# Kernel tuning notes

Measured on AMD Instinct MI355X. Metric: run time of the kernel, lower is better.

Reference implementation:

```python
import jax, jax.numpy as jnp
import numpy as np

WS = 8        # window_size
NH = 16       # num_heads

def setup_inputs() -> dict:
    key = jax.random.key(0)
    ks = jax.random.split(key, 6)
    B, H, W, C = 16, 64, 64, 512
    nW = (H // WS) * (W // WS)
    return {
        "x": jax.random.normal(ks[0], (B, H * W, C), jnp.float32),
        "qkv_w": jax.random.normal(ks[1], (3 * C, C), jnp.float32) * 0.02,
        "qkv_b": jax.random.normal(ks[2], (3 * C,), jnp.float32) * 0.02,
        "proj_w": jax.random.normal(ks[3], (C, C), jnp.float32) * 0.02,
        "proj_b": jax.random.normal(ks[4], (C,), jnp.float32) * 0.02,
        "attn_mask": jax.random.normal(ks[5], (nW, WS * WS, WS * WS), jnp.float32),
        "H": H,
        "W": W,
    }

def reference(x, qkv_w, qkv_b, proj_w, proj_b, attn_mask, H, W):
    B, N, C = x.shape
    ws = WS
    hd = C // NH
    scale = hd ** (-0.5)
    x_img = x.reshape(B, H, W, C)
    pad_h = (ws - H % ws) % ws
    pad_w = (ws - W % ws) % ws
    if pad_h > 0 or pad_w > 0:
        x_img = jnp.pad(x_img, ((0, 0), (0, pad_h), (0, pad_w), (0, 0)))
    Hp, Wp = H + pad_h, W + pad_w
    nW = (Hp // ws) * (Wp // ws)
    # window partition: [B*nW, ws*ws, C]
    x_win = x_img.reshape(B, Hp // ws, ws, Wp // ws, ws, C)
    x_win = x_win.transpose(0, 1, 3, 2, 4, 5).reshape(B * nW, ws * ws, C)
    # fused qkv projection (torch Linear: y = x @ W^T + b)
    qkv = x_win @ qkv_w.T + qkv_b
    qkv = qkv.reshape(B * nW, ws * ws, 3, NH, hd).transpose(2, 0, 3, 1, 4)
    q, k, v = qkv[0], qkv[1], qkv[2]  # each [B*nW, NH, ws*ws, hd]
    attn = jnp.einsum('bhqd,bhkd->bhqk', q, k) * scale
    if attn_mask is not None:
        attn = attn.reshape(B, nW, NH, ws * ws, ws * ws)
        attn = attn + attn_mask[None, :, None, :, :]
        attn = attn.reshape(B * nW, NH, ws * ws, ws * ws)
    attn = jax.nn.softmax(attn, axis=-1)
    out = jnp.einsum('bhqk,bhkd->bhqd', attn, v)
    out = out.transpose(0, 2, 1, 3).reshape(B * nW, ws * ws, C)
    out = out @ proj_w.T + proj_b
    # window reverse
    out = out.reshape(B, Hp // ws, Wp // ws, ws, ws, C)
    out = out.transpose(0, 1, 3, 2, 4, 5).reshape(B, Hp, Wp, C)
    out = out[:, :H, :W, :].reshape(B, H * W, C)
    return out
```

## Files before the change

kernel.cpp:

```cpp
#include <hip/hip_runtime.h>


typedef unsigned short u16;
typedef unsigned int u32;
typedef __attribute__((ext_vector_type(8))) u16 u16x8;
typedef __attribute__((ext_vector_type(8))) short short8;
typedef __attribute__((ext_vector_type(4))) float f32x4;

__device__ __forceinline__ u16 f2bf(float f) {
    u32 u = __float_as_uint(f);
    u += 0x7fffu + ((u >> 16) & 1u);
    return (u16)(u >> 16);
}

__device__ __forceinline__ f32x4 MFMA(u16x8 a, u16x8 b, f32x4 c) {
    return __builtin_amdgcn_mfma_f32_16x16x32_bf16(
        __builtin_bit_cast(short8, a), __builtin_bit_cast(short8, b), c, 0, 0, 0);
}

__device__ __forceinline__ void gload16(const void* g, void* l) {
    __builtin_amdgcn_global_load_lds(
        (const __attribute__((address_space(1))) void*)g,
        (__attribute__((address_space(3))) void*)l, 16, 0, 0);
}

__device__ __forceinline__ int win2img(int r) {
    int b = r >> 12;
    int w = (r >> 6) & 63;
    int t = r & 63;
    int img = (((w >> 3) << 3) + (t >> 3)) * 64 + ((w & 7) << 3) + (t & 7);
    return (b << 12) + img;
}

__device__ __forceinline__ u16x8 cvt8(const float* src) {
    float4 a = *(const float4*)src;
    float4 b = *(const float4*)(src + 4);
    u16x8 t;
    t[0] = f2bf(a.x); t[1] = f2bf(a.y); t[2] = f2bf(a.z); t[3] = f2bf(a.w);
    t[4] = f2bf(b.x); t[5] = f2bf(b.y); t[6] = f2bf(b.z); t[7] = f2bf(b.w);
    return t;
}

__global__ __launch_bounds__(256)
void conv_f2b(const float* __restrict__ in, u16* __restrict__ out, int n8) {
    int u = blockIdx.x * 256 + threadIdx.x;
    if (u >= n8) return;
    *(u16x8*)(out + (size_t)u * 8) = cvt8(in + (size_t)u * 8);
}

__global__ __launch_bounds__(256)
void conv_permute_x(const float* __restrict__ x, u16* __restrict__ xw) {
    int u = blockIdx.x * 256 + threadIdx.x;
    int r = u >> 6;
    int c = (u & 63) << 3;
    int g = win2img(r);
    *(u16x8*)(xw + (size_t)r * 512 + c) = cvt8(x + (size_t)g * 512 + c);
}

template<bool PERM_OUT, bool OUT_F32>
__global__ __launch_bounds__(256, 2)
void gemm_bt(const u16* __restrict__ A, const u16* __restrict__ Wt,
             const float* __restrict__ bias, void* __restrict__ C, int Nfull)
{
    __shared__ u16 sA[128 * 32];
    __shared__ u16 sB[128 * 32];

    const int tid  = threadIdx.x;
    const int lane = tid & 63;
    const int wv   = tid >> 6;
    const int wm   = (wv >> 1) << 6;
    const int wn   = (wv & 1) << 6;
    const int lr   = lane & 15;
    const int lg   = lane >> 4;
    const int m0   = blockIdx.x * 128;
    const int n0   = blockIdx.y * 128;

    const int grow  = tid >> 2;
    const int gcolb = (tid & 3) << 4;
    const u32 tb    = (u32)tid * 16;

    const char* aptr = (const char*)A + (((size_t)(m0 + grow)) << 10) + gcolb;
    const char* bptr = (const char*)Wt + (((size_t)(n0 + grow)) << 10) + gcolb;
    char* sAb = (char*)sA;
    char* sBb = (char*)sB;

    f32x4 acc[4][4] = {};

    for (int kt = 0; kt < 16; ++kt) {
        __syncthreads();
        const int ko = kt * 64;
        gload16(aptr + ko,              sAb + tb);
        gload16(aptr + (64 << 10) + ko, sAb + 4096 + tb);
        gload16(bptr + ko,              sBb + tb);
        gload16(bptr + (64 << 10) + ko, sBb + 4096 + tb);
        __syncthreads();

        u16x8 af[4], bfr[4];
#pragma unroll
        for (int mi = 0; mi < 4; ++mi)
            af[mi] = *(const u16x8*)(sA + (wm + mi * 16 + lr) * 32 + lg * 8);
#pragma unroll
        for (int ni = 0; ni < 4; ++ni)
            bfr[ni] = *(const u16x8*)(sB + (wn + ni * 16 + lr) * 32 + lg * 8);
#pragma unroll
        for (int mi = 0; mi < 4; ++mi)
#pragma unroll
            for (int ni = 0; ni < 4; ++ni)
                acc[mi][ni] = MFMA(af[mi], bfr[ni], acc[mi][ni]);
    }

#pragma unroll
    for (int mi = 0; mi < 4; ++mi) {
#pragma unroll
        for (int ni = 0; ni < 4; ++ni) {
            const int col = n0 + wn + ni * 16 + lr;
            const float bv = bias[col];
#pragma unroll
            for (int r = 0; r < 4; ++r) {
                int gr = m0 + wm + mi * 16 + lg * 4 + r;
                if (PERM_OUT) gr = win2img(gr);
                const float v = acc[mi][ni][r] + bv;
                if constexpr (OUT_F32)
                    ((float*)C)[(size_t)gr * Nfull + col] = v;
                else
                    ((u16*)C)[(size_t)gr * Nfull + col] = f2bf(v);
            }
        }
    }
}

__global__ __launch_bounds__(256, 2)
void attn_kernel(const u16* __restrict__ qkv, const float* __restrict__ mask,
                 u16* __restrict__ attn_out)
{
    __shared__ u16 sP[4][64][72];

    const int tid  = threadIdx.x;
    const int lane = tid & 63;
    const int wv   = tid >> 6;
    const int lr   = lane & 15;
    const int lg   = lane >> 4;
    const int win  = blockIdx.x;
    const int wib  = win & 63;
    const size_t rb = (size_t)win * 64;
    const float* maskp = mask + (size_t)wib * 64 * 64;
    const float scale = 0.17677669529663687f;

    for (int hi = 0; hi < 4; ++hi) {
        const int h = hi * 4 + wv;
        const size_t hoff = (size_t)h * 32;

        u16x8 qf[4], kf[4];
#pragma unroll
        for (int mt = 0; mt < 4; ++mt) {
            const u16* rowp = qkv + (rb + mt * 16 + lr) * 1536 + hoff + lg * 8;
            qf[mt] = *(const u16x8*)rowp;
            kf[mt] = *(const u16x8*)(rowp + 512);
        }
        f32x4 s[4][4] = {};
#pragma unroll
        for (int mi = 0; mi < 4; ++mi)
#pragma unroll
            for (int ni = 0; ni < 4; ++ni)
                s[mi][ni] = MFMA(qf[mi], kf[ni], s[mi][ni]);

        float rsum[4][4];
#pragma unroll
        for (int mi = 0; mi < 4; ++mi) {
#pragma unroll
            for (int r = 0; r < 4; ++r) {
                const int qrow = mi * 16 + lg * 4 + r;
                float vv[4];
                float mx = -1e30f;
#pragma unroll
                for (int ni = 0; ni < 4; ++ni) {
                    const int kcol = ni * 16 + lr;
                    float v = s[mi][ni][r] * scale + maskp[qrow * 64 + kcol];
                    vv[ni] = v;
                    mx = fmaxf(mx, v);
                }
#pragma unroll
                for (int mk = 1; mk <= 8; mk <<= 1)
                    mx = fmaxf(mx, __shfl_xor(mx, mk, 64));
                float sum = 0.f;
#pragma unroll
                for (int ni = 0; ni < 4; ++ni) {
                    float p = __expf(vv[ni] - mx);
                    sum += p;
                    s[mi][ni][r] = p;
                }
#pragma unroll
                for (int mk = 1; mk <= 8; mk <<= 1)
                    sum += __shfl_xor(sum, mk, 64);
                rsum[mi][r] = sum;
            }
        }

        __syncthreads();
#pragma unroll
        for (int mi = 0; mi < 4; ++mi)
#pragma unroll
            for (int ni = 0; ni < 4; ++ni)
#pragma unroll
                for (int r = 0; r < 4; ++r)
                    sP[wv][mi * 16 + lg * 4 + r][ni * 16 + lr] = f2bf(s[mi][ni][r]);
        __syncthreads();

        u16x8 pf[4][2];
#pragma unroll
        for (int mt = 0; mt < 4; ++mt)
#pragma unroll
            for (int k2 = 0; k2 < 2; ++k2)
                pf[mt][k2] = *(const u16x8*)&sP[wv][mt * 16 + lr][k2 * 32 + lg * 8];

        u16x8 vf[2][2];
#pragma unroll
        for (int k2 = 0; k2 < 2; ++k2)
#pragma unroll
            for (int nt = 0; nt < 2; ++nt) {
                const u16* vp = qkv + (rb + k2 * 32 + lg * 8) * 1536 + 1024 + hoff + nt * 16 + lr;
                u16x8 tmp;
#pragma unroll
                for (int j = 0; j < 8; ++j) tmp[j] = vp[(size_t)j * 1536];
                vf[k2][nt] = tmp;
            }

        f32x4 o[4][2] = {};
#pragma unroll
        for (int mt = 0; mt < 4; ++mt)
#pragma unroll
            for (int k2 = 0; k2 < 2; ++k2)
#pragma unroll
                for (int nt = 0; nt < 2; ++nt)
                    o[mt][nt] = MFMA(pf[mt][k2], vf[k2][nt], o[mt][nt]);

#pragma unroll
        for (int mt = 0; mt < 4; ++mt)
#pragma unroll
            for (int nt = 0; nt < 2; ++nt)
#pragma unroll
                for (int r = 0; r < 4; ++r) {
                    const int row = mt * 16 + lg * 4 + r;
                    const int d = nt * 16 + lr;
                    attn_out[(rb + row) * 512 + hoff + d] =
                        f2bf(o[mt][nt][r] / rsum[mt][r]);
                }
    }
}

extern "C" void kernel_launch(void* const* d_in, const int* in_sizes, int n_in,
                              void* d_out, int out_size, void* d_ws, size_t ws_size,
                              hipStream_t stream)
{
    const float* x      = (const float*)d_in[0];
    const float* qkv_w  = (const float*)d_in[1];
    const float* qkv_b  = (const float*)d_in[2];
    const float* proj_w = (const float*)d_in[3];
    const float* proj_b = (const float*)d_in[4];
    const float* mask   = (const float*)d_in[5];
    float* out = (float*)d_out;

    const size_t WQKV = 1536ull * 512;
    const size_t WPROJ = 512ull * 512;

    u16* wq = (u16*)d_ws;
    u16* wp = wq + WQKV;
    u16* chunk = wp + WPROJ;

    const size_t xwPB  = 4096ull * 512;
    const size_t qkvPB = 4096ull * 1536;
    const size_t attPB = 4096ull * 512;
    const size_t perBatchBytes = (xwPB + qkvPB + attPB) * 2;

    size_t avail = ws_size - (WQKV + WPROJ) * 2;
    int Bc = (int)(avail / perBatchBytes);
    if (Bc > 16) Bc = 16;
    if (Bc < 1) Bc = 1;

    u16* xw_ws  = chunk;
    u16* qkv_ws = xw_ws + (size_t)Bc * xwPB;
    u16* att_ws = qkv_ws + (size_t)Bc * qkvPB;

    conv_f2b<<<dim3((WQKV / 8 + 255) / 256), 256, 0, stream>>>(qkv_w, wq, (int)(WQKV / 8));
    conv_f2b<<<dim3((WPROJ / 8 + 255) / 256), 256, 0, stream>>>(proj_w, wp, (int)(WPROJ / 8));

    for (int b0 = 0; b0 < 16; b0 += Bc) {
        const int bc = (16 - b0) < Bc ? (16 - b0) : Bc;
        const float* xc = x + (size_t)b0 * 4096 * 512;
        float* outc = out + (size_t)b0 * 4096 * 512;

        conv_permute_x<<<dim3(bc * 1024), 256, 0, stream>>>(xc, xw_ws);
        gemm_bt<false, false><<<dim3(bc * 32, 12), 256, 0, stream>>>(
            xw_ws, wq, qkv_b, qkv_ws, 1536);
        attn_kernel<<<dim3(bc * 64), 256, 0, stream>>>(qkv_ws, mask, att_ws);
        gemm_bt<true, true><<<dim3(bc * 32, 4), 256, 0, stream>>>(
            att_ws, wp, proj_b, outc, 512);
    }
}
```

Baseline: 349.0 us.

## Double-buffer GEMM LDS tiles and remap blocks across XCDs with 1D grid

The GEMM kernel now double-buffers its A/B tiles in LDS, so the global-to-LDS load for the next k-step is issued before the MFMAs on the current one, and each step needs one barrier instead of two. The launch is flattened to a 1D grid, and block ids are remapped so that consecutive tiles land on the same XCD (blockIdx mod 8), which should improve L2 reuse of shared A rows. Launch bounds are raised to 4 waves-per-SIMD occupancy. This uses twice the LDS per block and adds register pressure, which could limit the higher occupancy target or cause spills. The remap assumes the grid size is divisible by 8.

Measured after the change: 332.0 us. 1.05x faster.

```diff
diff --git a/kernel.cpp b/kernel.cpp
--- a/kernel.cpp
+++ b/kernel.cpp
@@ -58,12 +58,18 @@
 }
 
 template<bool PERM_OUT, bool OUT_F32>
-__global__ __launch_bounds__(256, 2)
+__global__ __launch_bounds__(256, 4)
 void gemm_bt(const u16* __restrict__ A, const u16* __restrict__ Wt,
-             const float* __restrict__ bias, void* __restrict__ C, int Nfull)
+             const float* __restrict__ bias, void* __restrict__ C,
+             int NB, int Nfull)
 {
-    __shared__ u16 sA[128 * 32];
-    __shared__ u16 sB[128 * 32];
+    __shared__ char lds[32768];
+
+    const int nwg = gridDim.x;
+    const int q   = nwg >> 3;
+    const int wg  = (blockIdx.x & 7) * q + (blockIdx.x >> 3);
+    const int m0  = (wg / NB) * 128;
+    const int n0  = (wg % NB) * 128;
 
     const int tid  = threadIdx.x;
     const int lane = tid & 63;
@@ -72,42 +78,57 @@
     const int wn   = (wv & 1) << 6;
     const int lr   = lane & 15;
     const int lg   = lane >> 4;
-    const int m0   = blockIdx.x * 128;
-    const int n0   = blockIdx.y * 128;
 
     const int grow  = tid >> 2;
     const int gcolb = (tid & 3) << 4;
-    const u32 tb    = (u32)tid * 16;
+    const u32 tb    = (u32)tid << 4;
 
     const char* aptr = (const char*)A + (((size_t)(m0 + grow)) << 10) + gcolb;
     const char* bptr = (const char*)Wt + (((size_t)(n0 + grow)) << 10) + gcolb;
-    char* sAb = (char*)sA;
-    char* sBb = (char*)sB;
 
     f32x4 acc[4][4] = {};
 
-    for (int kt = 0; kt < 16; ++kt) {
+#define STAGE(buf, kt) do {                                                   \
+    const int ko_ = (kt) * 64;                                                \
+    char* d_ = lds + (buf) * 16384 + tb;                                      \
+    gload16(aptr + ko_,              d_);                                     \
+    gload16(aptr + (64 << 10) + ko_, d_ + 4096);                              \
+    gload16(bptr + ko_,              d_ + 8192);                              \
+    gload16(bptr + (64 << 10) + ko_, d_ + 12288);                             \
+} while (0)
+
+#define COMPUTE(buf) do {                                                     \
+    const u16* As_ = (const u16*)(lds + (buf) * 16384);                       \
+    const u16* Bs_ = (const u16*)(lds + (buf) * 16384 + 8192);                \
+    u16x8 af_[4], bf_[4];                                                     \
+    _Pragma("unroll")                                                         \
+    for (int mi = 0; mi < 4; ++mi)                                            \
+        af_[mi] = *(const u16x8*)(As_ + (wm + mi * 16 + lr) * 32 + lg * 8);   \
+    _Pragma("unroll")                                                         \
+    for (int ni = 0; ni < 4; ++ni)                                            \
+        bf_[ni] = *(const u16x8*)(Bs_ + (wn + ni * 16 + lr) * 32 + lg * 8);   \
+    _Pragma("unroll")                                                         \
+    for (int mi = 0; mi < 4; ++mi)                                            \
+        _Pragma("unroll")                                                     \
+        for (int ni = 0; ni < 4; ++ni)                                        \
+            acc[mi][ni] = MFMA(af_[mi], bf_[ni], acc[mi][ni]);                \
+} while (0)
+
+    STAGE(0, 0);
+    __syncthreads();
+
+#pragma unroll 1
+    for (int kt = 0; kt < 16; kt += 2) {
+        STAGE(1, kt + 1);
+        COMPUTE(0);
         __syncthreads();
-        const int ko = kt * 64;
-        gload16(aptr + ko,              sAb + tb);
-        gload16(aptr + (64 << 10) + ko, sAb + 4096 + tb);
-        gload16(bptr + ko,              sBb + tb);
-        gload16(bptr + (64 << 10) + ko, sBb + 4096 + tb);
+        if (kt + 2 < 16) STAGE(0, kt + 2);
+        COMPUTE(1);
         __syncthreads();
-
-        u16x8 af[4], bfr[4];
-#pragma unroll
-        for (int mi = 0; mi < 4; ++mi)
-            af[mi] = *(const u16x8*)(sA + (wm + mi * 16 + lr) * 32 + lg * 8);
-#pragma unroll
-        for (int ni = 0; ni < 4; ++ni)
-            bfr[ni] = *(const u16x8*)(sB + (wn + ni * 16 + lr) * 32 + lg * 8);
-#pragma unroll
-        for (int mi = 0; mi < 4; ++mi)
-#pragma unroll
-            for (int ni = 0; ni < 4; ++ni)
-                acc[mi][ni] = MFMA(af[mi], bfr[ni], acc[mi][ni]);
     }
+
+#undef STAGE
+#undef COMPUTE
 
 #pragma unroll
     for (int mi = 0; mi < 4; ++mi) {
@@ -260,7 +281,7 @@
     const float* mask   = (const float*)d_in[5];
     float* out = (float*)d_out;
 
-    const size_t WQKV = 1536ull * 512;
+    const size_t WQKV  = 1536ull * 512;
     const size_t WPROJ = 512ull * 512;
 
     u16* wq = (u16*)d_ws;
@@ -290,10 +311,10 @@
         float* outc = out + (size_t)b0 * 4096 * 512;
 
         conv_permute_x<<<dim3(bc * 1024), 256, 0, stream>>>(xc, xw_ws);
-        gemm_bt<false, false><<<dim3(bc * 32, 12), 256, 0, stream>>>(
-            xw_ws, wq, qkv_b, qkv_ws, 1536);
+        gemm_bt<false, false><<<dim3(bc * 32 * 12), 256, 0, stream>>>(
+            xw_ws, wq, qkv_b, qkv_ws, 12, 1536);
         attn_kernel<<<dim3(bc * 64), 256, 0, stream>>>(qkv_ws, mask, att_ws);
-        gemm_bt<true, true><<<dim3(bc * 32, 4), 256, 0, stream>>>(
-            att_ws, wp, proj_b, outc, 512);
+        gemm_bt<true, true><<<dim3(bc * 32 * 4), 256, 0, stream>>>(
+            att_ws, wp, proj_b, outc, 4, 512);
     }
 }
```

## Replace GEMM with 256x256 double-buffered 8-wave pipelined kernel

Applied to the files above, without the earlier changes.

Replaces the 128x128 single-buffered GEMM with a 512-thread kernel that computes 256x256 output tiles using K-step 64, double-buffered LDS (128KB) with XOR-swizzled layout, interleaved global-to-LDS prefetch and MFMA phases, s_setprio around MFMA bursts, and an XCD-aware block remap. The aim is to hide global load latency, cut the per-k-step syncthreads overhead, and raise data reuse per LDS byte. In exchange it runs at one block per CU with heavy register pressure (128 accumulators per lane), and the grid shrinks, which may reduce occupancy and leave tail imbalance.

Result: no change. 347.6 us (-0.4%).

```diff
diff --git a/kernel.cpp b/kernel.cpp
--- a/kernel.cpp
+++ b/kernel.cpp
@@ -58,66 +58,117 @@
 }
 
 template<bool PERM_OUT, bool OUT_F32>
-__global__ __launch_bounds__(256, 2)
-void gemm_bt(const u16* __restrict__ A, const u16* __restrict__ Wt,
-             const float* __restrict__ bias, void* __restrict__ C, int Nfull)
+__global__ __launch_bounds__(512, 1)
+void gemm8p(const u16* __restrict__ A, const u16* __restrict__ Wt,
+            const float* __restrict__ bias, void* __restrict__ C,
+            int NB, int Nfull)
 {
-    __shared__ u16 sA[128 * 32];
-    __shared__ u16 sB[128 * 32];
+    __shared__ char lds[131072];
+
+    const int nwg = gridDim.x;
+    const int q   = nwg >> 3;
+    const int wg  = ((int)blockIdx.x & 7) * q + ((int)blockIdx.x >> 3);
+    const int m0  = (wg / NB) * 256;
+    const int n0  = (wg % NB) * 256;
 
     const int tid  = threadIdx.x;
     const int lane = tid & 63;
     const int wv   = tid >> 6;
-    const int wm   = (wv >> 1) << 6;
-    const int wn   = (wv & 1) << 6;
-    const int lr   = lane & 15;
-    const int lg   = lane >> 4;
-    const int m0   = blockIdx.x * 128;
-    const int n0   = blockIdx.y * 128;
-
-    const int grow  = tid >> 2;
-    const int gcolb = (tid & 3) << 4;
-    const u32 tb    = (u32)tid * 16;
-
-    const char* aptr = (const char*)A + (((size_t)(m0 + grow)) << 10) + gcolb;
-    const char* bptr = (const char*)Wt + (((size_t)(n0 + grow)) << 10) + gcolb;
-    char* sAb = (char*)sA;
-    char* sBb = (char*)sB;
-
-    f32x4 acc[4][4] = {};
-
-    for (int kt = 0; kt < 16; ++kt) {
+    const int wm128 = (wv >> 2) << 7;
+    const int wn64  = (wv & 3) << 6;
+    const int lr = lane & 15;
+    const int lg = lane >> 4;
+
+    const int srow = tid >> 3;
+    const int gcol = (((tid & 7) ^ (srow & 7)) << 4);
+    const char* Ag = (const char*)A + (((size_t)(m0 + srow)) << 10) + gcol;
+    const char* Bg = (const char*)Wt + (((size_t)(n0 + srow)) << 10) + gcol;
+    const u32 stb = (u32)tid << 4;
+
+    const int colx = (lr & 7) << 4;
+    const u32 aro = (u32)(wm128 + lr) << 7;
+    const u32 bro = (u32)(wn64 + lr) << 7;
+
+    f32x4 acc[8][4] = {};
+    u16x8 af[4], bf[4];
+
+#define STG(buf, OP, h, kt) do {                                              \
+    const char* g_ = (OP) ? Bg : Ag;                                          \
+    char* d_ = lds + (buf) * 65536 + (OP) * 32768 + (h) * 16384 + stb;        \
+    gload16(g_ + ((size_t)((h) * 128) << 10) + ((kt) << 7), d_);              \
+    gload16(g_ + ((size_t)((h) * 128 + 64) << 10) + ((kt) << 7), d_ + 8192);  \
+} while (0)
+
+#define RDA(buf, h, s) do {                                                   \
+    _Pragma("unroll") for (int j_ = 0; j_ < 4; ++j_)                          \
+        af[j_] = *(const u16x8*)(lds + (buf) * 65536 + aro                    \
+                   + (((h) * 4 + j_) << 11) + ((((s) << 6) + (lg << 4)) ^ colx)); \
+} while (0)
+
+#define RDB(buf, s) do {                                                      \
+    _Pragma("unroll") for (int n_ = 0; n_ < 4; ++n_)                          \
+        bf[n_] = *(const u16x8*)(lds + (buf) * 65536 + 32768 + bro            \
+                   + (n_ << 11) + ((((s) << 6) + (lg << 4)) ^ colx));         \
+} while (0)
+
+#define MM16(h) do {                                                          \
+    __builtin_amdgcn_s_setprio(1);                                            \
+    _Pragma("unroll") for (int j_ = 0; j_ < 4; ++j_)                          \
+        _Pragma("unroll") for (int n_ = 0; n_ < 4; ++n_)                      \
+            acc[(h) * 4 + j_][n_] = MFMA(af[j_], bf[n_], acc[(h) * 4 + j_][n_]); \
+    __builtin_amdgcn_s_setprio(0);                                            \
+} while (0)
+
+#define BAR() __builtin_amdgcn_s_barrier()
+#define LGK0() do { asm volatile("s_waitcnt lgkmcnt(0)" ::: "memory");        \
+                    __builtin_amdgcn_sched_barrier(0); } while (0)
+
+    STG(0, 0, 0, 0); STG(0, 0, 1, 0); STG(0, 1, 0, 0); STG(0, 1, 1, 0);
+    __syncthreads();
+
+#pragma unroll
+    for (int it = 0; it < 4; ++it) {
+        const int t1 = 2 * it + 1, t2 = 2 * it + 2;
+        RDA(0, 0, 0); RDB(0, 0);
+        STG(1, 0, 0, t1); STG(1, 1, 0, t1);
+        BAR(); LGK0(); MM16(0); BAR();
+        RDA(0, 1, 0);
+        STG(1, 0, 1, t1); STG(1, 1, 1, t1);
+        BAR(); LGK0(); MM16(1); BAR();
+        RDA(0, 0, 1); RDB(0, 1);
+        BAR(); LGK0(); MM16(0); BAR();
+        RDA(0, 1, 1);
+        BAR(); LGK0(); MM16(1);
         __syncthreads();
-        const int ko = kt * 64;
-        gload16(aptr + ko,              sAb + tb);
-        gload16(aptr + (64 << 10) + ko, sAb + 4096 + tb);
-        gload16(bptr + ko,              sBb + tb);
-        gload16(bptr + (64 << 10) + ko, sBb + 4096 + tb);
+        RDA(1, 0, 0); RDB(1, 0);
+        if (it < 3) { STG(0, 0, 0, t2); STG(0, 1, 0, t2); }
+        BAR(); LGK0(); MM16(0); BAR();
+        RDA(1, 1, 0);
+        if (it < 3) { STG(0, 0, 1, t2); STG(0, 1, 1, t2); }
+        BAR(); LGK0(); MM16(1); BAR();
+        RDA(1, 0, 1); RDB(1, 1);
+        BAR(); LGK0(); MM16(0); BAR();
+        RDA(1, 1, 1);
+        BAR(); LGK0(); MM16(1);
         __syncthreads();
-
-        u16x8 af[4], bfr[4];
-#pragma unroll
-        for (int mi = 0; mi < 4; ++mi)
-            af[mi] = *(const u16x8*)(sA + (wm + mi * 16 + lr) * 32 + lg * 8);
-#pragma unroll
-        for (int ni = 0; ni < 4; ++ni)
-            bfr[ni] = *(const u16x8*)(sB + (wn + ni * 16 + lr) * 32 + lg * 8);
-#pragma unroll
-        for (int mi = 0; mi < 4; ++mi)
-#pragma unroll
-            for (int ni = 0; ni < 4; ++ni)
-                acc[mi][ni] = MFMA(af[mi], bfr[ni], acc[mi][ni]);
     }
 
-#pragma unroll
-    for (int mi = 0; mi < 4; ++mi) {
-#pragma unroll
-        for (int ni = 0; ni < 4; ++ni) {
-            const int col = n0 + wn + ni * 16 + lr;
-            const float bv = bias[col];
+#undef STG
+#undef RDA
+#undef RDB
+#undef MM16
+#undef BAR
+#undef LGK0
+
+#pragma unroll
+    for (int ni = 0; ni < 4; ++ni) {
+        const int col = n0 + wn64 + ni * 16 + lr;
+        const float bv = bias[col];
+#pragma unroll
+        for (int mi = 0; mi < 8; ++mi) {
 #pragma unroll
             for (int r = 0; r < 4; ++r) {
-                int gr = m0 + wm + mi * 16 + lg * 4 + r;
+                int gr = m0 + wm128 + mi * 16 + lg * 4 + r;
                 if (PERM_OUT) gr = win2img(gr);
                 const float v = acc[mi][ni][r] + bv;
                 if constexpr (OUT_F32)
@@ -260,7 +311,7 @@
     const float* mask   = (const float*)d_in[5];
     float* out = (float*)d_out;
 
-    const size_t WQKV = 1536ull * 512;
+    const size_t WQKV  = 1536ull * 512;
     const size_t WPROJ = 512ull * 512;
 
     u16* wq = (u16*)d_ws;
@@ -290,10 +341,10 @@
         float* outc = out + (size_t)b0 * 4096 * 512;
 
         conv_permute_x<<<dim3(bc * 1024), 256, 0, stream>>>(xc, xw_ws);
-        gemm_bt<false, false><<<dim3(bc * 32, 12), 256, 0, stream>>>(
-            xw_ws, wq, qkv_b, qkv_ws, 1536);
+        gemm8p<false, false><<<dim3(bc * 16 * 6), 512, 0, stream>>>(
+            xw_ws, wq, qkv_b, qkv_ws, 6, 1536);
         attn_kernel<<<dim3(bc * 64), 256, 0, stream>>>(qkv_ws, mask, att_ws);
-        gemm_bt<true, true><<<dim3(bc * 32, 4), 256, 0, stream>>>(
-            att_ws, wp, proj_b, outc, 512);
+        gemm8p<true, true><<<dim3(bc * 16 * 2), 512, 0, stream>>>(
+            att_ws, wp, proj_b, outc, 2, 512);
     }
 }
```
